# Kernel tuning notes

Hardware: AMD Instinct MI355X
Metric: run time of the kernel (lower is better)

Reference implementation:

```python
import jax, jax.numpy as jnp
import numpy as np
from jax.scipy.special import logsumexp

B, N, C = 64, 1024, 558
NUM_ITERS = 20
TEMP = 1.0
CLASS_W = 1.0
ASSIGN_W = 0.5
NEG_INF = -1e30  # grad-safe stand-in for float('-inf') used by the torch code
EPS = 1e-8


def setup_inputs() -> dict:
    key = jax.random.key(0)
    k1, k2, k3, k4 = jax.random.split(key, 4)
    logits = jax.random.normal(k1, (B, N, C), dtype=jnp.float32)
    labels = jax.random.randint(k2, (B, N), 0, C, dtype=jnp.int32)
    visible_mask = jax.random.uniform(k3, (B, N)) < 0.9
    visible_mask = visible_mask.at[:, 0].set(True)  # every worm has >=1 visible node
    dustbin_score = jnp.asarray(-1.0, dtype=jnp.float32)  # nn.Parameter(-1.0)
    return {"logits": logits, "dustbin_score": dustbin_score,
            "labels": labels, "visible_mask": visible_mask}


def _log_sinkhorn(log_scores, log_mu, log_nu, iters):
    # log_scores: [B, N, M]; log_mu: [B, N]; log_nu: [B, M]
    log_u0 = jnp.zeros(log_scores.shape[:2], jnp.float32)
    log_v0 = jnp.zeros((log_scores.shape[0], log_scores.shape[2]), jnp.float32)

    def step(carry, _):
        log_u, log_v = carry
        log_u = log_mu - logsumexp(log_scores + log_v[:, None, :], axis=-1)
        log_v = log_nu - logsumexp(log_scores + log_u[:, :, None], axis=1)
        return (log_u, log_v), None

    (log_u, log_v), _ = jax.lax.scan(step, (log_u0, log_v0), None, length=iters)
    return jnp.exp(log_scores + log_u[:, :, None] + log_v[:, None, :])


def reference(logits, dustbin_score, labels, visible_mask):
    log_probs = jax.nn.log_softmax(logits, axis=-1)  # [B, N, C]

    # ---- Matcher (one_to_one=False) ----
    log_scores = log_probs / TEMP
    dust = jnp.broadcast_to(dustbin_score / TEMP, (B, N, 1))
    ls = jnp.concatenate([log_scores, dust], axis=-1)  # [B, N, C+1]

    maskf = visible_mask.astype(jnp.float32)
    nvis = maskf.sum(axis=1)  # [B], >= 1 by construction
    log_mu = jnp.where(visible_mask, -jnp.log(nvis)[:, None], NEG_INF)  # [B, N]
    log_nu = jnp.full((B, C + 1), -jnp.log(jnp.float32(C + 1)))  # uniform marginals

    P = _log_sinkhorn(ls, log_mu, log_nu, NUM_ITERS)  # [B, N, C+1]
    soft = P[:, :, :-1]  # drop dustbin column -> [B, N, C]

    # ---- classification loss (worm-averaged NLL, label_smoothing=0) ----
    # labels are packed at the front: visible node with rank r uses labels[b, r]
    ranks = jnp.clip(jnp.cumsum(visible_mask.astype(jnp.int32), axis=1) - 1, 0)
    tgt = jnp.take_along_axis(labels, ranks, axis=1)  # [B, N]
    nll = -jnp.take_along_axis(log_probs, tgt[..., None], axis=2)[..., 0]  # [B, N]
    class_loss = ((nll * maskf).sum(axis=1) / nvis).mean()

    # ---- assignment confidence loss (worm-averaged entropy) ----
    ent = -(soft * jnp.log(soft + EPS)).sum(axis=-1)  # [B, N]
    assignment_loss = ((ent * maskf).sum(axis=1) / nvis).mean()

    total_loss = CLASS_W * class_loss + ASSIGN_W * assignment_loss
    return total_loss


if __name__ == "__main__":
    print(reference(**setup_inputs()))
```

## Files before the change

### kernel.cpp

```cpp
#include <hip/hip_runtime.h>
#include <hip/hip_fp16.h>

#define Bb 64
#define Nn 1024
#define Cc 558
#define CP1 559
#define CPAD 560
#define ITERS 20
#define PBLK 8
#define RPB (Nn/PBLK)
#define WAVES 8
#define RPW (RPB/WAVES)
#define BLOCK 512

struct __align__(16) H8 { __half2 a, b, c, d; };

__device__ __forceinline__ float wave_sum(float v) {
#pragma unroll
    for (int off = 32; off > 0; off >>= 1) v += __shfl_xor(v, off, 64);
    return v;
}

__global__ void k_detect(const unsigned int* __restrict__ mw, int* __restrict__ flag) {
    __shared__ int fF, fB;
    if (threadIdx.x == 0) { fF = 0; fB = 0; }
    __syncthreads();
    for (int i = threadIdx.x; i < (Bb * Nn) / 4; i += blockDim.x) {
        unsigned w = mw[i];
        if (w == 0x3F800000u) fF = 1;
        else if (w > 1u) fB = 1;
    }
    __syncthreads();
    if (threadIdx.x == 0) *flag = fF ? 2 : (fB ? 1 : 0);
}

__global__ __launch_bounds__(256) void k0_softmax(const float* __restrict__ logits,
        __half* __restrict__ p0, float* __restrict__ lse) {
    const int wave = threadIdx.x >> 6, lane = threadIdx.x & 63;
    const int r = (blockIdx.x << 2) + wave;
    const float* row = logits + (size_t)r * Cc;
    float e[8], e8 = 0.f, s = 0.f;
#pragma unroll
    for (int k = 0; k < 8; ++k) { e[k] = __expf(row[(k << 6) + lane]); s += e[k]; }
    if (lane < 46) { e8 = __expf(row[512 + lane]); s += e8; }
    s = wave_sum(s);
    const float inv = 1.f / s;
    __half* pr = p0 + (size_t)r * CPAD;
#pragma unroll
    for (int k = 0; k < 8; ++k) pr[(k << 6) + lane] = __float2half(e[k] * inv);
    if (lane < 46) pr[512 + lane] = __float2half(e8 * inv);
    if (lane == 0) lse[r] = __logf(s);
}

__global__ __launch_bounds__(256) void k1_batch(const float* __restrict__ logits,
        const int* __restrict__ labels, const void* __restrict__ maskp,
        const float* __restrict__ lse, const float* __restrict__ dustbin,
        float* __restrict__ class_part, float* __restrict__ inv_nvis,
        unsigned char* __restrict__ visc, float* __restrict__ dustp,
        const int* __restrict__ flag) {
    const int b = blockIdx.x, tid = threadIdx.x;
    const int mode = *flag;
    __shared__ int cs[256];
    __shared__ float red[256];
    int v[4]; int local = 0;
#pragma unroll
    for (int j = 0; j < 4; ++j) {
        const int n = tid * 4 + j;
        const int idx = b * Nn + n;
        int m;
        if (mode == 1)      m = ((const unsigned char*)maskp)[idx] != 0;
        else if (mode == 2) m = ((const float*)maskp)[idx] != 0.f;
        else                m = ((const int*)maskp)[idx] != 0;
        v[j] = m; local += m;
    }
    cs[tid] = local;
    __syncthreads();
    for (int off = 1; off < 256; off <<= 1) {
        int x = 0;
        if (tid >= off) x = cs[tid - off];
        __syncthreads();
        cs[tid] += x;
        __syncthreads();
    }
    const int nvis = cs[255];
    int run = cs[tid] - local;
    float nllsum = 0.f;
#pragma unroll
    for (int j = 0; j < 4; ++j) {
        const int n = tid * 4 + j;
        run += v[j];
        visc[b * Nn + n] = (unsigned char)v[j];
        if (v[j]) {
            const int rank = run - 1;
            const int tgt = labels[b * Nn + rank];
            nllsum += lse[b * Nn + n] - logits[((size_t)(b * Nn + n)) * Cc + tgt];
        }
    }
    red[tid] = nllsum;
    __syncthreads();
    for (int off = 128; off > 0; off >>= 1) {
        if (tid < off) red[tid] += red[tid + off];
        __syncthreads();
    }
    if (tid == 0) {
        class_part[b] = red[0] / (float)nvis;
        inv_nvis[b] = 1.f / (float)nvis;
        if (b == 0) *dustp = __expf(dustbin[0]);
    }
}

__global__ __launch_bounds__(BLOCK) void k2_iter(const __half* __restrict__ p0,
        const unsigned char* __restrict__ visc, const float* __restrict__ inv_nvis,
        const float* __restrict__ dustp_p, float* __restrict__ eu_arr,
        const float* __restrict__ Rp, float* __restrict__ Wp, const int first) {
    __shared__ float evl[CP1];
    __shared__ float partl[WAVES][CPAD];
    const int b = blockIdx.x >> 3, p = blockIdx.x & 7, tid = threadIdx.x;
    for (int c = tid; c < CP1; c += BLOCK) {
        float ev = 1.f;
        if (!first) {
            float s = 0.f;
#pragma unroll
            for (int q = 0; q < PBLK; ++q) s += Rp[(size_t)((b * PBLK + q) * CPAD) + c];
            ev = 1.f / (559.f * s);
        }
        evl[c] = ev;
    }
    __syncthreads();
    const int wave = tid >> 6, lane = tid & 63;
    float evr[8];
#pragma unroll
    for (int k = 0; k < 8; ++k) evr[k] = evl[(lane << 3) + k];
    const float evt = (lane < 46) ? evl[512 + lane] : 0.f;
    const float evd = evl[558];
    const float dustp = *dustp_p;
    const float invn = inv_nvis[b];
    float pc[8] = {0.f, 0.f, 0.f, 0.f, 0.f, 0.f, 0.f, 0.f};
    float pct = 0.f, pcd = 0.f;
    const int row0 = b * Nn + p * RPB + wave * RPW;
    for (int i = 0; i < RPW; ++i) {
        const int r = row0 + i;
        if (!visc[r]) { if (lane == 0) eu_arr[r] = 0.f; continue; }
        const __half* pr = p0 + (size_t)r * CPAD;
        const H8 hv = *(const H8*)(pr + (lane << 3));
        const float x0 = __low2float(hv.a), x1 = __high2float(hv.a);
        const float x2 = __low2float(hv.b), x3 = __high2float(hv.b);
        const float x4 = __low2float(hv.c), x5 = __high2float(hv.c);
        const float x6 = __low2float(hv.d), x7 = __high2float(hv.d);
        const float xt = (lane < 46) ? __half2float(pr[512 + lane]) : 0.f;
        float s = x0*evr[0] + x1*evr[1] + x2*evr[2] + x3*evr[3]
                + x4*evr[4] + x5*evr[5] + x6*evr[6] + x7*evr[7] + xt*evt;
        s = wave_sum(s);
        s += dustp * evd;
        const float euv = invn / s;
        if (lane == 0) eu_arr[r] = euv;
        pc[0] += x0*euv; pc[1] += x1*euv; pc[2] += x2*euv; pc[3] += x3*euv;
        pc[4] += x4*euv; pc[5] += x5*euv; pc[6] += x6*euv; pc[7] += x7*euv;
        pct += xt * euv; pcd += euv;
    }
#pragma unroll
    for (int k = 0; k < 8; ++k) partl[wave][(lane << 3) + k] = pc[k];
    if (lane < 46) partl[wave][512 + lane] = pct;
    if (lane == 0) partl[wave][558] = pcd * dustp;
    __syncthreads();
    for (int c = tid; c < CP1; c += BLOCK) {
        float s = 0.f;
#pragma unroll
        for (int w = 0; w < WAVES; ++w) s += partl[w][c];
        Wp[(size_t)((b * PBLK + p) * CPAD) + c] = s;
    }
}

__global__ __launch_bounds__(BLOCK) void k3_final(const __half* __restrict__ p0,
        const float* __restrict__ eu_arr, const float* __restrict__ Rp,
        const float* __restrict__ inv_nvis, float* __restrict__ assign_part) {
    __shared__ float evl[CP1];
    __shared__ float red[WAVES];
    const int b = blockIdx.x >> 3, p = blockIdx.x & 7, tid = threadIdx.x;
    for (int c = tid; c < CP1; c += BLOCK) {
        float s = 0.f;
#pragma unroll
        for (int q = 0; q < PBLK; ++q) s += Rp[(size_t)((b * PBLK + q) * CPAD) + c];
        evl[c] = 1.f / (559.f * s);
    }
    __syncthreads();
    const int wave = tid >> 6, lane = tid & 63;
    float evr[8];
#pragma unroll
    for (int k = 0; k < 8; ++k) evr[k] = evl[(lane << 3) + k];
    const float evt = (lane < 46) ? evl[512 + lane] : 0.f;
    float acc = 0.f;
    const int row0 = b * Nn + p * RPB + wave * RPW;
    for (int i = 0; i < RPW; ++i) {
        const int r = row0 + i;
        const float euv = eu_arr[r];
        if (euv == 0.f) continue;
        const __half* pr = p0 + (size_t)r * CPAD;
        const H8 hv = *(const H8*)(pr + (lane << 3));
        const float x0 = __low2float(hv.a), x1 = __high2float(hv.a);
        const float x2 = __low2float(hv.b), x3 = __high2float(hv.b);
        const float x4 = __low2float(hv.c), x5 = __high2float(hv.c);
        const float x6 = __low2float(hv.d), x7 = __high2float(hv.d);
        const float xt = (lane < 46) ? __half2float(pr[512 + lane]) : 0.f;
        float P;
        P = x0*euv*evr[0]; acc -= P * __logf(P + 1e-8f);
        P = x1*euv*evr[1]; acc -= P * __logf(P + 1e-8f);
        P = x2*euv*evr[2]; acc -= P * __logf(P + 1e-8f);
        P = x3*euv*evr[3]; acc -= P * __logf(P + 1e-8f);
        P = x4*euv*evr[4]; acc -= P * __logf(P + 1e-8f);
        P = x5*euv*evr[5]; acc -= P * __logf(P + 1e-8f);
        P = x6*euv*evr[6]; acc -= P * __logf(P + 1e-8f);
        P = x7*euv*evr[7]; acc -= P * __logf(P + 1e-8f);
        P = xt*euv*evt;    acc -= P * __logf(P + 1e-8f);
    }
    acc = wave_sum(acc);
    if (lane == 0) red[wave] = acc;
    __syncthreads();
    if (tid == 0) {
        float s = 0.f;
#pragma unroll
        for (int w = 0; w < WAVES; ++w) s += red[w];
        assign_part[blockIdx.x] = s * inv_nvis[b];
    }
}

__global__ void k4_out(const float* __restrict__ class_part,
                       const float* __restrict__ assign_part, float* __restrict__ out) {
    const int b = threadIdx.x;
    float v = class_part[b];
    float a = 0.f;
#pragma unroll
    for (int p = 0; p < PBLK; ++p) a += assign_part[b * PBLK + p];
    v += 0.5f * a;
    v = wave_sum(v);
    if (b == 0) out[0] = v * (1.f / 64.f);
}

extern "C" void kernel_launch(void* const* d_in, const int* in_sizes, int n_in,
                              void* d_out, int out_size, void* d_ws, size_t ws_size,
                              hipStream_t stream) {
    const float* logits = (const float*)d_in[0];
    const float* dustbin = (const float*)d_in[1];
    const int* labels = (const int*)d_in[2];
    const void* mask = d_in[3];
    float* out = (float*)d_out;

    char* ws = (char*)d_ws;
    size_t off = 0;
    __half* p0 = (__half*)(ws + off);          off += (size_t)Bb * Nn * CPAD * 2;
    float* lse = (float*)(ws + off);           off += (size_t)Bb * Nn * 4;
    float* eu = (float*)(ws + off);            off += (size_t)Bb * Nn * 4;
    unsigned char* visc = (unsigned char*)(ws + off); off += (size_t)Bb * Nn;
    float* inv_nvis = (float*)(ws + off);      off += Bb * 4;
    float* parts = (float*)(ws + off);         off += 2ull * Bb * PBLK * CPAD * 4;
    float* class_part = (float*)(ws + off);    off += Bb * 4;
    float* assign_part = (float*)(ws + off);   off += Bb * PBLK * 4;
    float* dustp = (float*)(ws + off);         off += 16;
    int* flag = (int*)(ws + off);              off += 16;
    const size_t SLOT = (size_t)Bb * PBLK * CPAD;

    k_detect<<<1, 256, 0, stream>>>((const unsigned int*)mask, flag);
    k0_softmax<<<(Bb * Nn) / 4, 256, 0, stream>>>(logits, p0, lse);
    k1_batch<<<Bb, 256, 0, stream>>>(logits, labels, mask, lse, dustbin,
                                     class_part, inv_nvis, visc, dustp, flag);
    for (int t = 0; t < ITERS; ++t) {
        float* Wb = parts + (size_t)(t & 1) * SLOT;
        const float* Rb = parts + (size_t)((t + 1) & 1) * SLOT;
        k2_iter<<<Bb * PBLK, BLOCK, 0, stream>>>(p0, visc, inv_nvis, dustp, eu, Rb, Wb,
                                                 (t == 0) ? 1 : 0);
    }
    k3_final<<<Bb * PBLK, BLOCK, 0, stream>>>(p0, eu,
            parts + (size_t)((ITERS - 1) & 1) * SLOT, inv_nvis, assign_part);
    k4_out<<<1, 64, 0, stream>>>(class_part, assign_part, out);
    (void)in_sizes; (void)n_in; (void)out_size; (void)ws_size;
}
```

Baseline: 463.1 us.

## Fuse softmax, Sinkhorn iterations and entropy into one persistent register-resident kernel

Replaces the per-iteration kernel launches with one persistent kernel of 256 blocks (4 per batch). Each wave keeps its 32 softmax rows as fp16 in registers, so the half-precision probability matrix is no longer re-read from global memory each iteration. Blocks of the same batch synchronise every iteration through an atomic counter with spin polling and a poll cap. The separate mask-detect and softmax kernels are folded in, and the class loss now adds logsumexp sums computed in the main kernel. This relies on all blocks being co-resident and uses many registers, which risks spills or a deadlock if the grid cannot be fully resident.

Result: slower. 976.4 us (+110.9%).

```diff
diff --git a/kernel.cpp b/kernel.cpp
--- a/kernel.cpp
+++ b/kernel.cpp
@@ -7,13 +7,16 @@
 #define CP1 559
 #define CPAD 560
 #define ITERS 20
-#define PBLK 8
-#define RPB (Nn/PBLK)
+#define BLKS_PER_B 4
 #define WAVES 8
-#define RPW (RPB/WAVES)
-#define BLOCK 512
-
-struct __align__(16) H8 { __half2 a, b, c, d; };
+#define RPW 32
+#define POLL_CAP (1 << 22)
+
+#if __has_builtin(__builtin_amdgcn_rcpf)
+#define RCP(x) __builtin_amdgcn_rcpf(x)
+#else
+#define RCP(x) (1.0f / (x))
+#endif
 
 __device__ __forceinline__ float wave_sum(float v) {
 #pragma unroll
@@ -21,47 +24,36 @@
     return v;
 }
 
-__global__ void k_detect(const unsigned int* __restrict__ mw, int* __restrict__ flag) {
-    __shared__ int fF, fB;
-    if (threadIdx.x == 0) { fF = 0; fB = 0; }
-    __syncthreads();
-    for (int i = threadIdx.x; i < (Bb * Nn) / 4; i += blockDim.x) {
-        unsigned w = mw[i];
-        if (w == 0x3F800000u) fF = 1;
-        else if (w > 1u) fB = 1;
-    }
-    __syncthreads();
-    if (threadIdx.x == 0) *flag = fF ? 2 : (fB ? 1 : 0);
-}
-
-__global__ __launch_bounds__(256) void k0_softmax(const float* __restrict__ logits,
-        __half* __restrict__ p0, float* __restrict__ lse) {
-    const int wave = threadIdx.x >> 6, lane = threadIdx.x & 63;
-    const int r = (blockIdx.x << 2) + wave;
-    const float* row = logits + (size_t)r * Cc;
-    float e[8], e8 = 0.f, s = 0.f;
-#pragma unroll
-    for (int k = 0; k < 8; ++k) { e[k] = __expf(row[(k << 6) + lane]); s += e[k]; }
-    if (lane < 46) { e8 = __expf(row[512 + lane]); s += e8; }
-    s = wave_sum(s);
-    const float inv = 1.f / s;
-    __half* pr = p0 + (size_t)r * CPAD;
-#pragma unroll
-    for (int k = 0; k < 8; ++k) pr[(k << 6) + lane] = __float2half(e[k] * inv);
-    if (lane < 46) pr[512 + lane] = __float2half(e8 * inv);
-    if (lane == 0) lse[r] = __logf(s);
+__device__ __forceinline__ void g_store(float* p, float v) {
+    __hip_atomic_store(p, v, __ATOMIC_RELAXED, __HIP_MEMORY_SCOPE_AGENT);
+}
+__device__ __forceinline__ float g_load(const float* p) {
+    return __hip_atomic_load(p, __ATOMIC_RELAXED, __HIP_MEMORY_SCOPE_AGENT);
 }
 
 __global__ __launch_bounds__(256) void k1_batch(const float* __restrict__ logits,
         const int* __restrict__ labels, const void* __restrict__ maskp,
-        const float* __restrict__ lse, const float* __restrict__ dustbin,
-        float* __restrict__ class_part, float* __restrict__ inv_nvis,
-        unsigned char* __restrict__ visc, float* __restrict__ dustp,
-        const int* __restrict__ flag) {
+        float* __restrict__ A_part, float* __restrict__ inv_nvis,
+        unsigned char* __restrict__ visc, int* __restrict__ ctr) {
     const int b = blockIdx.x, tid = threadIdx.x;
-    const int mode = *flag;
-    __shared__ int cs[256];
+    __shared__ int sF, sB;
+    __shared__ int cs_[256];
     __shared__ float red[256];
+    if (tid == 0) { sF = 0; sB = 0; }
+    __syncthreads();
+    {
+        const unsigned int* mw = (const unsigned int*)maskp;
+        int lF = 0, lB = 0;
+        for (int i = tid; i < (Bb * Nn) / 4; i += 256) {
+            unsigned w = mw[i];
+            if (w == 0x3F800000u) lF = 1;
+            else if (w > 1u) lB = 1;
+        }
+        if (lF) sF = 1;
+        if (lB) sB = 1;
+    }
+    __syncthreads();
+    const int mode = sF ? 2 : (sB ? 1 : 0);
     int v[4]; int local = 0;
 #pragma unroll
     for (int j = 0; j < 4; ++j) {
@@ -73,17 +65,17 @@
         else                m = ((const int*)maskp)[idx] != 0;
         v[j] = m; local += m;
     }
-    cs[tid] = local;
+    cs_[tid] = local;
     __syncthreads();
     for (int off = 1; off < 256; off <<= 1) {
         int x = 0;
-        if (tid >= off) x = cs[tid - off];
-        __syncthreads();
-        cs[tid] += x;
-        __syncthreads();
-    }
-    const int nvis = cs[255];
-    int run = cs[tid] - local;
+        if (tid >= off) x = cs_[tid - off];
+        __syncthreads();
+        cs_[tid] += x;
+        __syncthreads();
+    }
+    const int nvis = cs_[255];
+    int run = cs_[tid] - local;
     float nllsum = 0.f;
 #pragma unroll
     for (int j = 0; j < 4; ++j) {
@@ -91,9 +83,8 @@
         run += v[j];
         visc[b * Nn + n] = (unsigned char)v[j];
         if (v[j]) {
-            const int rank = run - 1;
-            const int tgt = labels[b * Nn + rank];
-            nllsum += lse[b * Nn + n] - logits[((size_t)(b * Nn + n)) * Cc + tgt];
+            const int tgt = labels[b * Nn + (run - 1)];
+            nllsum -= logits[((size_t)(b * Nn + n)) * Cc + tgt];
         }
     }
     red[tid] = nllsum;
@@ -103,135 +94,185 @@
         __syncthreads();
     }
     if (tid == 0) {
-        class_part[b] = red[0] / (float)nvis;
+        A_part[b] = red[0];
         inv_nvis[b] = 1.f / (float)nvis;
-        if (b == 0) *dustp = __expf(dustbin[0]);
-    }
-}
-
-__global__ __launch_bounds__(BLOCK) void k2_iter(const __half* __restrict__ p0,
+        __hip_atomic_store(&ctr[b], 0, __ATOMIC_RELAXED, __HIP_MEMORY_SCOPE_AGENT);
+    }
+}
+
+__global__ __launch_bounds__(512, 2) void k_main(
+        const float* __restrict__ logits, const float* __restrict__ dustbin,
         const unsigned char* __restrict__ visc, const float* __restrict__ inv_nvis,
-        const float* __restrict__ dustp_p, float* __restrict__ eu_arr,
-        const float* __restrict__ Rp, float* __restrict__ Wp, const int first) {
-    __shared__ float evl[CP1];
+        float* __restrict__ cs, int* __restrict__ ctr, float* __restrict__ eu_g,
+        float* __restrict__ lse_part, float* __restrict__ ent_part) {
     __shared__ float partl[WAVES][CPAD];
-    const int b = blockIdx.x >> 3, p = blockIdx.x & 7, tid = threadIdx.x;
-    for (int c = tid; c < CP1; c += BLOCK) {
-        float ev = 1.f;
-        if (!first) {
-            float s = 0.f;
-#pragma unroll
-            for (int q = 0; q < PBLK; ++q) s += Rp[(size_t)((b * PBLK + q) * CPAD) + c];
-            ev = 1.f / (559.f * s);
-        }
-        evl[c] = ev;
-    }
-    __syncthreads();
-    const int wave = tid >> 6, lane = tid & 63;
-    float evr[8];
-#pragma unroll
-    for (int k = 0; k < 8; ++k) evr[k] = evl[(lane << 3) + k];
-    const float evt = (lane < 46) ? evl[512 + lane] : 0.f;
-    const float evd = evl[558];
-    const float dustp = *dustp_p;
+    __shared__ float evl[CPAD];
+    __shared__ float redL[WAVES], redE[WAVES];
+    const int g = blockIdx.x;
+    const int b = ((g & 7) << 3) | (g >> 5);
+    const int p = (g >> 3) & 3;
+    const int tid = threadIdx.x, wave = tid >> 6, lane = tid & 63;
+    const int row0 = (b << 10) + (p << 8) + (wave << 5);
+    const float dustp = __expf(dustbin[0]);
     const float invn = inv_nvis[b];
-    float pc[8] = {0.f, 0.f, 0.f, 0.f, 0.f, 0.f, 0.f, 0.f};
-    float pct = 0.f, pcd = 0.f;
-    const int row0 = b * Nn + p * RPB + wave * RPW;
-    for (int i = 0; i < RPW; ++i) {
-        const int r = row0 + i;
-        if (!visc[r]) { if (lane == 0) eu_arr[r] = 0.f; continue; }
-        const __half* pr = p0 + (size_t)r * CPAD;
-        const H8 hv = *(const H8*)(pr + (lane << 3));
-        const float x0 = __low2float(hv.a), x1 = __high2float(hv.a);
-        const float x2 = __low2float(hv.b), x3 = __high2float(hv.b);
-        const float x4 = __low2float(hv.c), x5 = __high2float(hv.c);
-        const float x6 = __low2float(hv.d), x7 = __high2float(hv.d);
-        const float xt = (lane < 46) ? __half2float(pr[512 + lane]) : 0.f;
-        float s = x0*evr[0] + x1*evr[1] + x2*evr[2] + x3*evr[3]
-                + x4*evr[4] + x5*evr[5] + x6*evr[6] + x7*evr[7] + xt*evt;
-        s = wave_sum(s);
-        s += dustp * evd;
-        const float euv = invn / s;
-        if (lane == 0) eu_arr[r] = euv;
-        pc[0] += x0*euv; pc[1] += x1*euv; pc[2] += x2*euv; pc[3] += x3*euv;
-        pc[4] += x4*euv; pc[5] += x5*euv; pc[6] += x6*euv; pc[7] += x7*euv;
-        pct += xt * euv; pcd += euv;
-    }
-#pragma unroll
-    for (int k = 0; k < 8; ++k) partl[wave][(lane << 3) + k] = pc[k];
-    if (lane < 46) partl[wave][512 + lane] = pct;
-    if (lane == 0) partl[wave][558] = pcd * dustp;
-    __syncthreads();
-    for (int c = tid; c < CP1; c += BLOCK) {
-        float s = 0.f;
-#pragma unroll
-        for (int w = 0; w < WAVES; ++w) s += partl[w][c];
-        Wp[(size_t)((b * PBLK + p) * CPAD) + c] = s;
-    }
-}
-
-__global__ __launch_bounds__(BLOCK) void k3_final(const __half* __restrict__ p0,
-        const float* __restrict__ eu_arr, const float* __restrict__ Rp,
-        const float* __restrict__ inv_nvis, float* __restrict__ assign_part) {
-    __shared__ float evl[CP1];
-    __shared__ float red[WAVES];
-    const int b = blockIdx.x >> 3, p = blockIdx.x & 7, tid = threadIdx.x;
-    for (int c = tid; c < CP1; c += BLOCK) {
-        float s = 0.f;
-#pragma unroll
-        for (int q = 0; q < PBLK; ++q) s += Rp[(size_t)((b * PBLK + q) * CPAD) + c];
-        evl[c] = 1.f / (559.f * s);
-    }
-    __syncthreads();
-    const int wave = tid >> 6, lane = tid & 63;
-    float evr[8];
-#pragma unroll
-    for (int k = 0; k < 8; ++k) evr[k] = evl[(lane << 3) + k];
-    const float evt = (lane < 46) ? evl[512 + lane] : 0.f;
+    const int tl = lane < 46;
+
+    const uint4 vA = *(const uint4*)(visc + row0);
+    const uint4 vB = *(const uint4*)(visc + row0 + 16);
+    unsigned vw[8] = {vA.x, vA.y, vA.z, vA.w, vB.x, vB.y, vB.z, vB.w};
+#define VIS(r) ((vw[(r) >> 2] >> (((r) & 3) << 3)) & 0xffu)
+
+    __half2 px[RPW][4];
+    float pt[RPW];
+    float lsesum = 0.f;
+
+#pragma unroll
+    for (int r = 0; r < RPW; ++r) {
+        if (__builtin_amdgcn_readfirstlane(VIS(r))) {
+            const float* rowp = logits + (size_t)(row0 + r) * Cc;
+            const int c0 = lane << 3;
+            float e0 = __expf(rowp[c0 + 0]), e1 = __expf(rowp[c0 + 1]);
+            float e2 = __expf(rowp[c0 + 2]), e3 = __expf(rowp[c0 + 3]);
+            float e4 = __expf(rowp[c0 + 4]), e5 = __expf(rowp[c0 + 5]);
+            float e6 = __expf(rowp[c0 + 6]), e7 = __expf(rowp[c0 + 7]);
+            float et = tl ? __expf(rowp[512 + lane]) : 0.f;
+            float s = wave_sum(e0 + e1 + e2 + e3 + e4 + e5 + e6 + e7 + et);
+            const float inv = RCP(s);
+            px[r][0] = __floats2half2_rn(e0 * inv, e1 * inv);
+            px[r][1] = __floats2half2_rn(e2 * inv, e3 * inv);
+            px[r][2] = __floats2half2_rn(e4 * inv, e5 * inv);
+            px[r][3] = __floats2half2_rn(e6 * inv, e7 * inv);
+            pt[r] = et * inv;
+            lsesum += __logf(s);
+        } else {
+            px[r][0] = px[r][1] = px[r][2] = px[r][3] = __floats2half2_rn(0.f, 0.f);
+            pt[r] = 0.f;
+        }
+    }
+
+    float evr[8], evt, evd;
+    for (int t = 0; t < ITERS; ++t) {
+        if (t == 0) {
+#pragma unroll
+            for (int k = 0; k < 8; ++k) evr[k] = 1.f;
+            evt = 1.f; evd = 1.f;
+        } else {
+            const float* CSr = cs + (size_t)(((t - 1) & 1) * Bb + b) * (BLKS_PER_B * CPAD);
+            for (int c = tid; c < CP1; c += 512) {
+                float s = g_load(CSr + c) + g_load(CSr + CPAD + c)
+                        + g_load(CSr + 2 * CPAD + c) + g_load(CSr + 3 * CPAD + c);
+                evl[c] = RCP(559.f * s);
+            }
+            __syncthreads();
+#pragma unroll
+            for (int k = 0; k < 8; ++k) evr[k] = evl[(lane << 3) + k];
+            evt = tl ? evl[512 + lane] : 0.f;
+            evd = evl[558];
+        }
+        float pc0 = 0.f, pc1 = 0.f, pc2 = 0.f, pc3 = 0.f;
+        float pc4 = 0.f, pc5 = 0.f, pc6 = 0.f, pc7 = 0.f;
+        float pct = 0.f, pcd = 0.f;
+        const float dd = dustp * evd;
+#pragma unroll
+        for (int r = 0; r < RPW; ++r) {
+            if (__builtin_amdgcn_readfirstlane(VIS(r))) {
+                const float2 f0 = __half22float2(px[r][0]);
+                const float2 f1 = __half22float2(px[r][1]);
+                const float2 f2 = __half22float2(px[r][2]);
+                const float2 f3 = __half22float2(px[r][3]);
+                float s = pt[r] * evt
+                        + f0.x * evr[0] + f0.y * evr[1] + f1.x * evr[2] + f1.y * evr[3]
+                        + f2.x * evr[4] + f2.y * evr[5] + f3.x * evr[6] + f3.y * evr[7];
+                s = wave_sum(s) + dd;
+                const float euv = invn * RCP(s);
+                if (t == ITERS - 1 && lane == 0) eu_g[row0 + r] = euv;
+                pc0 += f0.x * euv; pc1 += f0.y * euv; pc2 += f1.x * euv; pc3 += f1.y * euv;
+                pc4 += f2.x * euv; pc5 += f2.y * euv; pc6 += f3.x * euv; pc7 += f3.y * euv;
+                pct += pt[r] * euv; pcd += euv;
+            } else if (t == ITERS - 1 && lane == 0) {
+                eu_g[row0 + r] = 0.f;
+            }
+        }
+        const int cb = lane << 3;
+        partl[wave][cb + 0] = pc0; partl[wave][cb + 1] = pc1;
+        partl[wave][cb + 2] = pc2; partl[wave][cb + 3] = pc3;
+        partl[wave][cb + 4] = pc4; partl[wave][cb + 5] = pc5;
+        partl[wave][cb + 6] = pc6; partl[wave][cb + 7] = pc7;
+        if (tl) partl[wave][512 + lane] = pct;
+        if (lane == 0) partl[wave][558] = pcd * dustp;
+        __syncthreads();
+        float* CSw = cs + ((size_t)((t & 1) * Bb + b) * BLKS_PER_B + p) * CPAD;
+        for (int c = tid; c < CP1; c += 512) {
+            float s = partl[0][c] + partl[1][c] + partl[2][c] + partl[3][c]
+                    + partl[4][c] + partl[5][c] + partl[6][c] + partl[7][c];
+            g_store(CSw + c, s);
+        }
+        __syncthreads();
+        if (tid == 0) {
+            __hip_atomic_fetch_add(&ctr[b], 1, __ATOMIC_RELEASE, __HIP_MEMORY_SCOPE_AGENT);
+            const int target = BLKS_PER_B * (t + 1);
+            int polls = 0;
+            while (__hip_atomic_load(&ctr[b], __ATOMIC_ACQUIRE, __HIP_MEMORY_SCOPE_AGENT) < target) {
+                __builtin_amdgcn_s_sleep(1);
+                if (++polls > POLL_CAP) break;
+            }
+        }
+        __syncthreads();
+    }
+
+    {
+        const float* CSr = cs + (size_t)(((ITERS - 1) & 1) * Bb + b) * (BLKS_PER_B * CPAD);
+        for (int c = tid; c < CP1; c += 512) {
+            float s = g_load(CSr + c) + g_load(CSr + CPAD + c)
+                    + g_load(CSr + 2 * CPAD + c) + g_load(CSr + 3 * CPAD + c);
+            evl[c] = RCP(559.f * s);
+        }
+        __syncthreads();
+#pragma unroll
+        for (int k = 0; k < 8; ++k) evr[k] = evl[(lane << 3) + k];
+        evt = tl ? evl[512 + lane] : 0.f;
+    }
     float acc = 0.f;
-    const int row0 = b * Nn + p * RPB + wave * RPW;
-    for (int i = 0; i < RPW; ++i) {
-        const int r = row0 + i;
-        const float euv = eu_arr[r];
-        if (euv == 0.f) continue;
-        const __half* pr = p0 + (size_t)r * CPAD;
-        const H8 hv = *(const H8*)(pr + (lane << 3));
-        const float x0 = __low2float(hv.a), x1 = __high2float(hv.a);
-        const float x2 = __low2float(hv.b), x3 = __high2float(hv.b);
-        const float x4 = __low2float(hv.c), x5 = __high2float(hv.c);
-        const float x6 = __low2float(hv.d), x7 = __high2float(hv.d);
-        const float xt = (lane < 46) ? __half2float(pr[512 + lane]) : 0.f;
-        float P;
-        P = x0*euv*evr[0]; acc -= P * __logf(P + 1e-8f);
-        P = x1*euv*evr[1]; acc -= P * __logf(P + 1e-8f);
-        P = x2*euv*evr[2]; acc -= P * __logf(P + 1e-8f);
-        P = x3*euv*evr[3]; acc -= P * __logf(P + 1e-8f);
-        P = x4*euv*evr[4]; acc -= P * __logf(P + 1e-8f);
-        P = x5*euv*evr[5]; acc -= P * __logf(P + 1e-8f);
-        P = x6*euv*evr[6]; acc -= P * __logf(P + 1e-8f);
-        P = x7*euv*evr[7]; acc -= P * __logf(P + 1e-8f);
-        P = xt*euv*evt;    acc -= P * __logf(P + 1e-8f);
+#pragma unroll
+    for (int r = 0; r < RPW; ++r) {
+        if (__builtin_amdgcn_readfirstlane(VIS(r))) {
+            const float euv = eu_g[row0 + r];
+            const float2 f0 = __half22float2(px[r][0]);
+            const float2 f1 = __half22float2(px[r][1]);
+            const float2 f2 = __half22float2(px[r][2]);
+            const float2 f3 = __half22float2(px[r][3]);
+            float P;
+            P = f0.x * euv * evr[0]; acc -= P * __logf(P + 1e-8f);
+            P = f0.y * euv * evr[1]; acc -= P * __logf(P + 1e-8f);
+            P = f1.x * euv * evr[2]; acc -= P * __logf(P + 1e-8f);
+            P = f1.y * euv * evr[3]; acc -= P * __logf(P + 1e-8f);
+            P = f2.x * euv * evr[4]; acc -= P * __logf(P + 1e-8f);
+            P = f2.y * euv * evr[5]; acc -= P * __logf(P + 1e-8f);
+            P = f3.x * euv * evr[6]; acc -= P * __logf(P + 1e-8f);
+            P = f3.y * euv * evr[7]; acc -= P * __logf(P + 1e-8f);
+            P = pt[r] * euv * evt;   acc -= P * __logf(P + 1e-8f);
+        }
     }
     acc = wave_sum(acc);
-    if (lane == 0) red[wave] = acc;
+    if (lane == 0) { redE[wave] = acc; redL[wave] = lsesum; }
     __syncthreads();
     if (tid == 0) {
-        float s = 0.f;
-#pragma unroll
-        for (int w = 0; w < WAVES; ++w) s += red[w];
-        assign_part[blockIdx.x] = s * inv_nvis[b];
-    }
-}
-
-__global__ void k4_out(const float* __restrict__ class_part,
-                       const float* __restrict__ assign_part, float* __restrict__ out) {
+        float eS = 0.f, lS = 0.f;
+#pragma unroll
+        for (int w = 0; w < WAVES; ++w) { eS += redE[w]; lS += redL[w]; }
+        ent_part[(b << 2) | p] = eS;
+        lse_part[(b << 2) | p] = lS;
+    }
+}
+
+__global__ void k4_out(const float* __restrict__ A_part, const float* __restrict__ lse_part,
+        const float* __restrict__ ent_part, const float* __restrict__ inv_nvis,
+        float* __restrict__ out) {
     const int b = threadIdx.x;
-    float v = class_part[b];
-    float a = 0.f;
-#pragma unroll
-    for (int p = 0; p < PBLK; ++p) a += assign_part[b * PBLK + p];
-    v += 0.5f * a;
+    float l = 0.f, e = 0.f;
+#pragma unroll
+    for (int p = 0; p < 4; ++p) { l += lse_part[(b << 2) | p]; e += ent_part[(b << 2) | p]; }
+    float v = (A_part[b] + l) * inv_nvis[b] + 0.5f * e * inv_nvis[b];
     v = wave_sum(v);
     if (b == 0) out[0] = v * (1.f / 64.f);
 }
@@ -247,30 +288,18 @@
 
     char* ws = (char*)d_ws;
     size_t off = 0;
-    __half* p0 = (__half*)(ws + off);          off += (size_t)Bb * Nn * CPAD * 2;
-    float* lse = (float*)(ws + off);           off += (size_t)Bb * Nn * 4;
-    float* eu = (float*)(ws + off);            off += (size_t)Bb * Nn * 4;
+    float* cs = (float*)(ws + off);            off += 2ull * Bb * BLKS_PER_B * CPAD * 4;
+    int* ctr = (int*)(ws + off);               off += Bb * 4;
+    float* eu_g = (float*)(ws + off);          off += (size_t)Bb * Nn * 4;
     unsigned char* visc = (unsigned char*)(ws + off); off += (size_t)Bb * Nn;
     float* inv_nvis = (float*)(ws + off);      off += Bb * 4;
-    float* parts = (float*)(ws + off);         off += 2ull * Bb * PBLK * CPAD * 4;
-    float* class_part = (float*)(ws + off);    off += Bb * 4;
-    float* assign_part = (float*)(ws + off);   off += Bb * PBLK * 4;
-    float* dustp = (float*)(ws + off);         off += 16;
-    int* flag = (int*)(ws + off);              off += 16;
-    const size_t SLOT = (size_t)Bb * PBLK * CPAD;
-
-    k_detect<<<1, 256, 0, stream>>>((const unsigned int*)mask, flag);
-    k0_softmax<<<(Bb * Nn) / 4, 256, 0, stream>>>(logits, p0, lse);
-    k1_batch<<<Bb, 256, 0, stream>>>(logits, labels, mask, lse, dustbin,
-                                     class_part, inv_nvis, visc, dustp, flag);
-    for (int t = 0; t < ITERS; ++t) {
-        float* Wb = parts + (size_t)(t & 1) * SLOT;
-        const float* Rb = parts + (size_t)((t + 1) & 1) * SLOT;
-        k2_iter<<<Bb * PBLK, BLOCK, 0, stream>>>(p0, visc, inv_nvis, dustp, eu, Rb, Wb,
-                                                 (t == 0) ? 1 : 0);
-    }
-    k3_final<<<Bb * PBLK, BLOCK, 0, stream>>>(p0, eu,
-            parts + (size_t)((ITERS - 1) & 1) * SLOT, inv_nvis, assign_part);
-    k4_out<<<1, 64, 0, stream>>>(class_part, assign_part, out);
+    float* A_part = (float*)(ws + off);        off += Bb * 4;
+    float* lse_part = (float*)(ws + off);      off += Bb * BLKS_PER_B * 4;
+    float* ent_part = (float*)(ws + off);      off += Bb * BLKS_PER_B * 4;
+
+    k1_batch<<<Bb, 256, 0, stream>>>(logits, labels, mask, A_part, inv_nvis, visc, ctr);
+    k_main<<<Bb * BLKS_PER_B, 512, 0, stream>>>(logits, dustbin, visc, inv_nvis,
+                                                cs, ctr, eu_g, lse_part, ent_part);
+    k4_out<<<1, 64, 0, stream>>>(A_part, lse_part, ent_part, inv_nvis, out);
     (void)in_sizes; (void)n_in; (void)out_size; (void)ws_size;
 }
```
